# Kernel tuning notes

Measured on AMD Instinct MI355X. Metric: run time of the kernel, lower is better.

## Reference

```python
import jax, jax.numpy as jnp
import numpy as np

D_MODEL = 1024
N_HEADS = 16
HEAD_DIM = D_MODEL // N_HEADS  # 64
BASE = 10000.0
MAX_X, MAX_Y, MAX_Z = 32, 32, 8
NEG_INF = -1e9  # stand-in for float('-inf') in masked_fill; identical after softmax


def _split_dims(head_dim):
    n_pairs = head_dim // 2
    px = n_pairs // 3
    py = n_pairs // 3
    pz = n_pairs - px - py
    return px * 2, py * 2, pz * 2


def _cos_sin_table(dim, max_pos):
    # matches RotaryEmbedding3D._register_cache
    inv_freq = 1.0 / (BASE ** (np.arange(0, dim, 2, dtype=np.float32) / dim))
    t = np.arange(max_pos, dtype=np.float32)[:, None] * inv_freq  # [max_pos, dim/2]
    cos = np.repeat(np.cos(t), 2, axis=-1)  # repeat_interleave(2)
    sin = np.repeat(np.sin(t), 2, axis=-1)
    return jnp.asarray(cos), jnp.asarray(sin)


def _rotate_half(x):
    x1 = x[..., ::2]
    x2 = x[..., 1::2]
    return jnp.stack((-x2, x1), axis=-1).reshape(x.shape)


def setup_inputs() -> dict:
    key = jax.random.key(0)
    k1, k2, k3, k4, k5, k6 = jax.random.split(key, 6)
    B, S = 2, 2048
    hidden_states = jax.random.normal(k1, (B, S, D_MODEL), dtype=jnp.float32)
    w_qkv = jax.random.normal(k2, (D_MODEL, 3 * D_MODEL), dtype=jnp.float32) * 0.02
    w_out = jax.random.normal(k3, (D_MODEL, D_MODEL), dtype=jnp.float32) * 0.02
    px = jax.random.randint(k4, (B, S, 1), 0, MAX_X)
    py = jax.random.randint(k5, (B, S, 1), 0, MAX_Y)
    pz = jax.random.randint(k6, (B, S, 1), 0, MAX_Z)
    pos_xyz = jnp.concatenate([px, py, pz], axis=-1).astype(jnp.int64)
    causal_mask = jnp.triu(jnp.ones((S, S), dtype=bool), k=1)[None, None]  # [1,1,S,S]
    return {"hidden_states": hidden_states, "w_qkv": w_qkv, "w_out": w_out,
            "pos_xyz": pos_xyz, "causal_mask": causal_mask}


def reference(hidden_states, w_qkv, w_out, pos_xyz, causal_mask):
    B, S, D = hidden_states.shape
    H, Hd = N_HEADS, HEAD_DIM
    # fused QKV projection
    qkv = hidden_states @ w_qkv  # [B,S,3D]
    qkv = qkv.reshape(B, S, 3, H, Hd).transpose(2, 0, 3, 1, 4)  # [3,B,H,S,Hd]
    q, k, v = qkv[0], qkv[1], qkv[2]
    # 3D RoPE tables and lookups
    dx, dy, dz = _split_dims(Hd)
    cx, sx = _cos_sin_table(dx, MAX_X)
    cy, sy = _cos_sin_table(dy, MAX_Y)
    cz, sz = _cos_sin_table(dz, MAX_Z)
    ix = jnp.clip(pos_xyz[..., 0], 0, MAX_X - 1)
    iy = jnp.clip(pos_xyz[..., 1], 0, MAX_Y - 1)
    iz = jnp.clip(pos_xyz[..., 2], 0, MAX_Z - 1)
    cos = jnp.concatenate([cx[ix], cy[iy], cz[iz]], axis=-1)[:, None]  # [B,1,S,Hd]
    sin = jnp.concatenate([sx[ix], sy[iy], sz[iz]], axis=-1)[:, None]
    q = q * cos + _rotate_half(q) * sin
    k = k * cos + _rotate_half(k) * sin
    # SDPA with causal bias
    scale = Hd ** -0.5
    scores = jnp.einsum('bhqd,bhkd->bhqk', q, k) * scale
    scores = jnp.where(causal_mask, jnp.asarray(NEG_INF, scores.dtype), scores)
    probs = jax.nn.softmax(scores, axis=-1)
    attn = jnp.einsum('bhqk,bhkd->bhqd', probs, v)
    attn = attn.transpose(0, 2, 1, 3).reshape(B, S, D)
    return attn @ w_out
```

## Files before the change

### kernel.cpp

```cpp
#include <hip/hip_runtime.h>
#include <hip/hip_bf16.h>
#include <math.h>

typedef __bf16 bf16;
typedef __bf16 bf16x8 __attribute__((ext_vector_type(8)));
typedef float f32x4 __attribute__((ext_vector_type(4)));

#define SEQ 2048
#define NHEADS 16
#define HDIM 64
#define DM 1024
#define QKVW 3072

__device__ __forceinline__ void gload_lds16(const void* g, void* l) {
  __builtin_amdgcn_global_load_lds(
      (const __attribute__((address_space(1))) unsigned int*)g,
      (__attribute__((address_space(3))) unsigned int*)l, 16, 0, 0);
}

template <int CTRL>
__device__ __forceinline__ float dppmovf(float x) {
  return __builtin_bit_cast(
      float, __builtin_amdgcn_mov_dpp(__builtin_bit_cast(int, x), CTRL, 0xf,
                                      0xf, true));
}
__device__ __forceinline__ float rowsum16(float x) {
  x += dppmovf<0xB1>(x);
  x += dppmovf<0x4E>(x);
  x += dppmovf<0x124>(x);
  x += dppmovf<0x128>(x);
  return x;
}

__global__ __launch_bounds__(256) void prep(
    const float* __restrict__ hidden, const float* __restrict__ w_qkv,
    const float* __restrict__ w_out, const int* __restrict__ pos,
    bf16* __restrict__ hid_bf, bf16* __restrict__ wqkvT,
    bf16* __restrict__ woutT, float2* __restrict__ tbl) {
  __shared__ float tile[64][65];
  int idx = blockIdx.x, tid = threadIdx.x;
  if (idx < 2048) {
    int i = (idx * 256 + tid) * 8;
    float4 a = *(const float4*)(hidden + i);
    float4 b = *(const float4*)(hidden + i + 4);
    bf16x8 o;
    o[0] = (bf16)a.x; o[1] = (bf16)a.y; o[2] = (bf16)a.z; o[3] = (bf16)a.w;
    o[4] = (bf16)b.x; o[5] = (bf16)b.y; o[6] = (bf16)b.z; o[7] = (bf16)b.w;
    *(bf16x8*)(hid_bf + i) = o;
  } else if (idx < 3072) {
    const float* in; bf16* out; int R, C, t;
    if (idx < 2816) { t = idx - 2048; in = w_qkv; out = wqkvT; R = 1024; C = 3072; }
    else            { t = idx - 2816; in = w_out; out = woutT; R = 1024; C = 1024; }
    int nbx = C >> 6;
    int c0 = (t % nbx) * 64, r0 = (t / nbx) * 64;
    int col = tid & 63, rb = (tid >> 6) * 16;
#pragma unroll
    for (int i = 0; i < 16; ++i)
      tile[rb + i][col] = in[(size_t)(r0 + rb + i) * C + c0 + col];
    __syncthreads();
#pragma unroll
    for (int i = 0; i < 16; ++i)
      out[(size_t)(c0 + rb + i) * R + r0 + col] = (bf16)tile[col][rb + i];
  } else {
    const float LN1E4 = 9.210340371976184f;
    int gi = (idx - 3072) * 256 + tid;
    int m = gi >> 5, pr = gi & 31;
    int axis, d, iloc;
    if (pr < 10)      { axis = 0; d = 20; iloc = pr; }
    else if (pr < 20) { axis = 1; d = 20; iloc = pr - 10; }
    else              { axis = 2; d = 24; iloc = pr - 20; }
    int p = pos[m * 3 + axis];
    int pmax = (axis == 2) ? 7 : 31;
    p = p < 0 ? 0 : (p > pmax ? pmax : p);
    float invf = __expf(-((float)(2 * iloc) / (float)d) * LN1E4);
    float sn, cs;
    __sincosf((float)p * invf, &sn, &cs);
    tbl[gi] = make_float2(cs, sn);
  }
}

__global__ __launch_bounds__(256) void post_qkv(
    bf16* __restrict__ qkv, const float2* __restrict__ tbl,
    bf16* __restrict__ vT) {
  __shared__ bf16 btile[64][65];
  int idx = blockIdx.x, tid = threadIdx.x;
  if (idx < 2048) {
    int gi = idx * 256 + tid;
    int m = gi >> 7, seg = gi & 127;
    bf16* p = qkv + (size_t)m * QKVW + seg * 16;
    bf16x8 a = *(const bf16x8*)p;
    bf16x8 b2 = *(const bf16x8*)(p + 8);
    const float2* t = tbl + m * 32 + (((seg * 16) & 63) >> 1);
#pragma unroll
    for (int j = 0; j < 4; ++j) {
      float2 cs = t[j];
      float e = (float)a[2 * j], o = (float)a[2 * j + 1];
      a[2 * j]     = (bf16)(e * cs.x - o * cs.y);
      a[2 * j + 1] = (bf16)(o * cs.x + e * cs.y);
    }
#pragma unroll
    for (int j = 0; j < 4; ++j) {
      float2 cs = t[4 + j];
      float e = (float)b2[2 * j], o = (float)b2[2 * j + 1];
      b2[2 * j]     = (bf16)(e * cs.x - o * cs.y);
      b2[2 * j + 1] = (bf16)(o * cs.x + e * cs.y);
    }
    *(bf16x8*)p = a;
    *(bf16x8*)(p + 8) = b2;
  } else {
    int t = idx - 2048;
    int s0 = (t & 31) * 64, bh = t >> 5;
    int b = bh >> 4, h = bh & 15;
    const bf16* src = qkv + (size_t)(b * SEQ + s0) * QKVW + 2 * DM + h * 64;
    int col = tid & 63, rb = (tid >> 6) * 16;
#pragma unroll
    for (int i = 0; i < 16; ++i)
      btile[rb + i][col] = src[(size_t)(rb + i) * QKVW + col];
    __syncthreads();
    bf16* dst = vT + (size_t)bh * HDIM * SEQ + s0;
#pragma unroll
    for (int i = 0; i < 16; ++i)
      dst[(size_t)(rb + i) * SEQ + col] = btile[col][rb + i];
  }
}

__global__ __launch_bounds__(256) void gemm_bt(
    const bf16* __restrict__ A, const bf16* __restrict__ Bt,
    bf16* __restrict__ C, int M, int N, int K) {
  __shared__ __align__(16) bf16 a_lds[128 * 32];
  __shared__ __align__(16) bf16 b_lds[128 * 32];
  int tid = threadIdx.x;
  int wave = tid >> 6, lane = tid & 63;
  int quad = lane >> 4, l15 = lane & 15;
  int wm = wave >> 1, wn = wave & 1;

  int flat = blockIdx.y * gridDim.x + blockIdx.x;
  int mband = gridDim.y >> 3;
  int xcd = flat & 7, sidx = flat >> 3;
  int m0 = (xcd * mband + (sidx % mband)) * 128;
  int n0 = (sidx / mband) * 128;

  f32x4 acc[4][4] = {};

  for (int kt = 0; kt < K; kt += 32) {
    __syncthreads();
#pragma unroll
    for (int call = 0; call < 2; ++call) {
      int chunk = call * 256 + tid;
      int row = chunk >> 2, cc = (chunk & 3) * 8;
      gload_lds16(A + (size_t)(m0 + row) * K + kt + cc,
                  (char*)a_lds + call * 4096 + wave * 1024);
      gload_lds16(Bt + (size_t)(n0 + row) * K + kt + cc,
                  (char*)b_lds + call * 4096 + wave * 1024);
    }
    __syncthreads();
    bf16x8 af[4], bfr[4];
#pragma unroll
    for (int i = 0; i < 4; ++i) {
      af[i]  = *(const bf16x8*)(a_lds + (wm * 64 + i * 16 + l15) * 32 + quad * 8);
      bfr[i] = *(const bf16x8*)(b_lds + (wn * 64 + i * 16 + l15) * 32 + quad * 8);
    }
#pragma unroll
    for (int mi = 0; mi < 4; ++mi)
#pragma unroll
      for (int ni = 0; ni < 4; ++ni)
        acc[mi][ni] = __builtin_amdgcn_mfma_f32_16x16x32_bf16(
            af[mi], bfr[ni], acc[mi][ni], 0, 0, 0);
  }

#pragma unroll
  for (int mi = 0; mi < 4; ++mi) {
    int mb = m0 + wm * 64 + mi * 16 + quad * 4;
#pragma unroll
    for (int ni = 0; ni < 4; ++ni) {
      int n = n0 + wn * 64 + ni * 16 + l15;
#pragma unroll
      for (int r = 0; r < 4; ++r)
        C[(size_t)(mb + r) * N + n] = (bf16)acc[mi][ni][r];
    }
  }
}

__global__ __launch_bounds__(256) void gemm_bt64(
    const bf16* __restrict__ A, const bf16* __restrict__ Bt,
    float* __restrict__ C, int M, int N, int K) {
  __shared__ __align__(16) bf16 a_lds[64 * 32];
  __shared__ __align__(16) bf16 b_lds[128 * 32];
  int tid = threadIdx.x;
  int wave = tid >> 6, lane = tid & 63;
  int quad = lane >> 4, l15 = lane & 15;
  int wm = wave >> 1, wn = wave & 1;

  int flat = blockIdx.y * gridDim.x + blockIdx.x;
  int mband = gridDim.y >> 3;
  int xcd = flat & 7, sidx = flat >> 3;
  int m0 = (xcd * mband + (sidx % mband)) * 64;
  int n0 = (sidx / mband) * 128;

  f32x4 acc[2][4] = {};

  for (int kt = 0; kt < K; kt += 32) {
    __syncthreads();
    {
      int row = tid >> 2, cc = (tid & 3) * 8;
      gload_lds16(A + (size_t)(m0 + row) * K + kt + cc,
                  (char*)a_lds + wave * 1024);
    }
#pragma unroll
    for (int call = 0; call < 2; ++call) {
      int chunk = call * 256 + tid;
      int row = chunk >> 2, cc = (chunk & 3) * 8;
      gload_lds16(Bt + (size_t)(n0 + row) * K + kt + cc,
                  (char*)b_lds + call * 4096 + wave * 1024);
    }
    __syncthreads();
    bf16x8 af[2], bfr[4];
#pragma unroll
    for (int i = 0; i < 2; ++i)
      af[i] = *(const bf16x8*)(a_lds + (wm * 32 + i * 16 + l15) * 32 + quad * 8);
#pragma unroll
    for (int i = 0; i < 4; ++i)
      bfr[i] = *(const bf16x8*)(b_lds + (wn * 64 + i * 16 + l15) * 32 + quad * 8);
#pragma unroll
    for (int mi = 0; mi < 2; ++mi)
#pragma unroll
      for (int ni = 0; ni < 4; ++ni)
        acc[mi][ni] = __builtin_amdgcn_mfma_f32_16x16x32_bf16(
            af[mi], bfr[ni], acc[mi][ni], 0, 0, 0);
  }

#pragma unroll
  for (int mi = 0; mi < 2; ++mi) {
    int mb = m0 + wm * 32 + mi * 16 + quad * 4;
#pragma unroll
    for (int ni = 0; ni < 4; ++ni) {
      int n = n0 + wn * 64 + ni * 16 + l15;
#pragma unroll
      for (int r = 0; r < 4; ++r)
        C[(size_t)(mb + r) * N + n] = acc[mi][ni][r];
    }
  }
}

__global__ __launch_bounds__(256) void attn_fwd(
    const bf16* __restrict__ QKV, const bf16* __restrict__ VT,
    bf16* __restrict__ O) {
  __shared__ __align__(16) bf16 k_lds[2][64 * 72];
  __shared__ __align__(16) bf16 v_lds[2][64 * 72];
  __shared__ __align__(16) bf16 p_lds[4][16 * 72];
  const float C2 = 0.18033688011112042f;
  const float C3 = -5.770780163555854f;
  int tid = threadIdx.x;
  int wave = tid >> 6, lane = tid & 63;
  int quad = lane >> 4, l15 = lane & 15;
  int idx = blockIdx.x;
  int bh = idx & 31;
  int g = idx >> 5;
  int qt = (g < 16) ? (31 - g) : (g - 16);
  int q0 = qt * 64;
  int b = bh >> 4, h = bh & 15;
  const bf16* Qb = QKV + (size_t)b * SEQ * QKVW + h * 64;
  const bf16* Kb = Qb + DM;
  const bf16* VTb = VT + (size_t)bh * HDIM * SEQ;
  bf16* pw = p_lds[wave];

  const bf16* qr = Qb + (size_t)(q0 + wave * 16 + l15) * QKVW;
  bf16x8 qf0 = *(const bf16x8*)(qr + quad * 8);
  bf16x8 qf1 = *(const bf16x8*)(qr + 32 + quad * 8);

  int r0c = tid >> 3, off0 = (tid & 7) * 8;

  int niter = qt + 1;
  f32x4 o_acc[4] = {};
  float lsum[4] = {};
  int qrow[4];
#pragma unroll
  for (int r = 0; r < 4; ++r) qrow[r] = q0 + wave * 16 + quad * 4 + r;

  bf16x8 kpre0 = *(const bf16x8*)(Kb + (size_t)r0c * QKVW + off0);
  bf16x8 kpre1 = *(const bf16x8*)(Kb + (size_t)(r0c + 32) * QKVW + off0);
  bf16x8 vpre0 = *(const bf16x8*)(VTb + (size_t)r0c * SEQ + off0);
  bf16x8 vpre1 = *(const bf16x8*)(VTb + (size_t)(r0c + 32) * SEQ + off0);

  for (int tkv = 0; tkv < niter; ++tkv) {
    int kv0 = tkv * 64;
    bf16* kb = k_lds[tkv & 1];
    bf16* vb = v_lds[tkv & 1];
    *(bf16x8*)(kb + r0c * 72 + off0) = kpre0;
    *(bf16x8*)(kb + (r0c + 32) * 72 + off0) = kpre1;
    *(bf16x8*)(vb + r0c * 72 + off0) = vpre0;
    *(bf16x8*)(vb + (r0c + 32) * 72 + off0) = vpre1;
    __syncthreads();
    if (tkv + 1 < niter) {
      int kn = kv0 + 64;
      kpre0 = *(const bf16x8*)(Kb + (size_t)(kn + r0c) * QKVW + off0);
      kpre1 = *(const bf16x8*)(Kb + (size_t)(kn + r0c + 32) * QKVW + off0);
      vpre0 = *(const bf16x8*)(VTb + (size_t)r0c * SEQ + kn + off0);
      vpre1 = *(const bf16x8*)(VTb + (size_t)(r0c + 32) * SEQ + kn + off0);
    }
    f32x4 s_acc[4];
    __builtin_amdgcn_s_setprio(1);
#pragma unroll
    for (int nt = 0; nt < 4; ++nt) {
      const bf16* kr = kb + (nt * 16 + l15) * 72;
      bf16x8 kf0 = *(const bf16x8*)(kr + quad * 8);
      bf16x8 kf1 = *(const bf16x8*)(kr + 32 + quad * 8);
      f32x4 z = {};
      z = __builtin_amdgcn_mfma_f32_16x16x32_bf16(qf0, kf0, z, 0, 0, 0);
      z = __builtin_amdgcn_mfma_f32_16x16x32_bf16(qf1, kf1, z, 0, 0, 0);
      s_acc[nt] = z;
    }
    __builtin_amdgcn_s_setprio(0);
    if (tkv == qt) {
#pragma unroll
      for (int r = 0; r < 4; ++r) {
#pragma unroll
        for (int nt = 0; nt < 4; ++nt) {
          float p = __builtin_amdgcn_exp2f(s_acc[nt][r] * C2 + C3);
          if (kv0 + nt * 16 + l15 > qrow[r]) p = 0.f;
          lsum[r] += p;
          pw[(quad * 4 + r) * 72 + nt * 16 + l15] = (bf16)p;
        }
      }
    } else {
#pragma unroll
      for (int r = 0; r < 4; ++r) {
#pragma unroll
        for (int nt = 0; nt < 4; ++nt) {
          float p = __builtin_amdgcn_exp2f(s_acc[nt][r] * C2 + C3);
          lsum[r] += p;
          pw[(quad * 4 + r) * 72 + nt * 16 + l15] = (bf16)p;
        }
      }
    }
    __asm__ volatile("s_waitcnt lgkmcnt(0)" ::: "memory");
    bf16x8 pf0 = *(const bf16x8*)(pw + l15 * 72 + quad * 8);
    bf16x8 pf1 = *(const bf16x8*)(pw + l15 * 72 + 32 + quad * 8);
    __builtin_amdgcn_s_setprio(1);
#pragma unroll
    for (int nt = 0; nt < 4; ++nt) {
      const bf16* vr = vb + (nt * 16 + l15) * 72;
      bf16x8 vf0 = *(const bf16x8*)(vr + quad * 8);
      bf16x8 vf1 = *(const bf16x8*)(vr + 32 + quad * 8);
      o_acc[nt] = __builtin_amdgcn_mfma_f32_16x16x32_bf16(pf0, vf0, o_acc[nt], 0, 0, 0);
      o_acc[nt] = __builtin_amdgcn_mfma_f32_16x16x32_bf16(pf1, vf1, o_acc[nt], 0, 0, 0);
    }
    __builtin_amdgcn_s_setprio(0);
  }
#pragma unroll
  for (int r = 0; r < 4; ++r) {
    float inv = 1.f / rowsum16(lsum[r]);
    int sq = qrow[r];
#pragma unroll
    for (int nt = 0; nt < 4; ++nt)
      O[((size_t)(b * SEQ + sq)) * DM + h * HDIM + nt * 16 + l15] =
          (bf16)(o_acc[nt][r] * inv);
  }
}

extern "C" void kernel_launch(void* const* d_in, const int* in_sizes, int n_in,
                              void* d_out, int out_size, void* d_ws,
                              size_t ws_size, hipStream_t stream) {
  const float* hidden = (const float*)d_in[0];
  const float* w_qkv  = (const float*)d_in[1];
  const float* w_out  = (const float*)d_in[2];
  const int*   pos    = (const int*)d_in[3];
  float* out = (float*)d_out;

  char* ws = (char*)d_ws;
  bf16* wqkvT  = (bf16*)ws;  ws += (size_t)3072 * 1024 * 2;
  bf16* woutT  = (bf16*)ws;  ws += (size_t)1024 * 1024 * 2;
  bf16* hid_bf = (bf16*)ws;  ws += (size_t)4096 * 1024 * 2;
  bf16* qkv_ws = (bf16*)ws;  ws += (size_t)4096 * 3072 * 2;
  bf16* vT_ws  = (bf16*)ws;  ws += (size_t)32 * SEQ * HDIM * 2;
  float2* ropetbl = (float2*)ws;
  bf16* attn_ws = hid_bf;

  prep<<<dim3(3584), 256, 0, stream>>>(hidden, w_qkv, w_out, pos,
                                       hid_bf, wqkvT, woutT, ropetbl);
  gemm_bt<<<dim3(24, 32), 256, 0, stream>>>(
      hid_bf, wqkvT, qkv_ws, 4096, 3072, 1024);
  post_qkv<<<dim3(3072), 256, 0, stream>>>(qkv_ws, ropetbl, vT_ws);
  attn_fwd<<<dim3(1024), 256, 0, stream>>>(qkv_ws, vT_ws, attn_ws);
  gemm_bt64<<<dim3(8, 64), 256, 0, stream>>>(
      attn_ws, woutT, out, 4096, 1024, 1024);
}
```

Before: 200.1 us.

## Compute transposed scores to keep P in registers and skip the LDS round-trip

The QK^T MFMA now runs with its operands swapped, so each lane holds scores for one query across several keys. That layout lets the probabilities be packed straight into bf16 MFMA A-operands without writing P to shared memory and reading it back. V fragments are now read as split 4-element LDS loads to match the new k ordering, and the row-sum reduction moves from a DPP reduction to cross-quad shuffles. This removes per-tile LDS stores, a wait and reloads of P, at the cost of narrower V loads and possibly more bank conflicts.

Result: faster. 196.1 us (-2.0%).

```diff
diff --git a/kernel.cpp b/kernel.cpp
--- a/kernel.cpp
+++ b/kernel.cpp
@@ -3,8 +3,10 @@
 #include <math.h>
 
 typedef __bf16 bf16;
+typedef __bf16 bf16x4 __attribute__((ext_vector_type(4)));
 typedef __bf16 bf16x8 __attribute__((ext_vector_type(8)));
 typedef float f32x4 __attribute__((ext_vector_type(4)));
+typedef int i32x4 __attribute__((ext_vector_type(4)));
 
 #define SEQ 2048
 #define NHEADS 16
@@ -18,18 +20,10 @@
       (__attribute__((address_space(3))) unsigned int*)l, 16, 0, 0);
 }
 
-template <int CTRL>
-__device__ __forceinline__ float dppmovf(float x) {
-  return __builtin_bit_cast(
-      float, __builtin_amdgcn_mov_dpp(__builtin_bit_cast(int, x), CTRL, 0xf,
-                                      0xf, true));
-}
-__device__ __forceinline__ float rowsum16(float x) {
-  x += dppmovf<0xB1>(x);
-  x += dppmovf<0x4E>(x);
-  x += dppmovf<0x124>(x);
-  x += dppmovf<0x128>(x);
-  return x;
+__device__ __forceinline__ int pk2(float a, float b) {
+  union { __bf16 h; unsigned short u; } ua, ub;
+  ua.h = (__bf16)a; ub.h = (__bf16)b;
+  return (int)ua.u | ((int)ub.u << 16);
 }
 
 __global__ __launch_bounds__(256) void prep(
@@ -247,7 +241,6 @@
     bf16* __restrict__ O) {
   __shared__ __align__(16) bf16 k_lds[2][64 * 72];
   __shared__ __align__(16) bf16 v_lds[2][64 * 72];
-  __shared__ __align__(16) bf16 p_lds[4][16 * 72];
   const float C2 = 0.18033688011112042f;
   const float C3 = -5.770780163555854f;
   int tid = threadIdx.x;
@@ -262,20 +255,17 @@
   const bf16* Qb = QKV + (size_t)b * SEQ * QKVW + h * 64;
   const bf16* Kb = Qb + DM;
   const bf16* VTb = VT + (size_t)bh * HDIM * SEQ;
-  bf16* pw = p_lds[wave];
-
-  const bf16* qr = Qb + (size_t)(q0 + wave * 16 + l15) * QKVW;
+
+  int qg = q0 + wave * 16 + l15;
+  const bf16* qr = Qb + (size_t)qg * QKVW;
   bf16x8 qf0 = *(const bf16x8*)(qr + quad * 8);
   bf16x8 qf1 = *(const bf16x8*)(qr + 32 + quad * 8);
 
   int r0c = tid >> 3, off0 = (tid & 7) * 8;
 
   int niter = qt + 1;
-  f32x4 o_acc[4] = {};
-  float lsum[4] = {};
-  int qrow[4];
-#pragma unroll
-  for (int r = 0; r < 4; ++r) qrow[r] = q0 + wave * 16 + quad * 4 + r;
+  f32x4 oT[4] = {};
+  float lsum = 0.f;
 
   bf16x8 kpre0 = *(const bf16x8*)(Kb + (size_t)r0c * QKVW + off0);
   bf16x8 kpre1 = *(const bf16x8*)(Kb + (size_t)(r0c + 32) * QKVW + off0);
@@ -298,7 +288,7 @@
       vpre0 = *(const bf16x8*)(VTb + (size_t)r0c * SEQ + kn + off0);
       vpre1 = *(const bf16x8*)(VTb + (size_t)(r0c + 32) * SEQ + kn + off0);
     }
-    f32x4 s_acc[4];
+    f32x4 sT[4];
     __builtin_amdgcn_s_setprio(1);
 #pragma unroll
     for (int nt = 0; nt < 4; ++nt) {
@@ -306,55 +296,66 @@
       bf16x8 kf0 = *(const bf16x8*)(kr + quad * 8);
       bf16x8 kf1 = *(const bf16x8*)(kr + 32 + quad * 8);
       f32x4 z = {};
-      z = __builtin_amdgcn_mfma_f32_16x16x32_bf16(qf0, kf0, z, 0, 0, 0);
-      z = __builtin_amdgcn_mfma_f32_16x16x32_bf16(qf1, kf1, z, 0, 0, 0);
-      s_acc[nt] = z;
+      z = __builtin_amdgcn_mfma_f32_16x16x32_bf16(kf0, qf0, z, 0, 0, 0);
+      z = __builtin_amdgcn_mfma_f32_16x16x32_bf16(kf1, qf1, z, 0, 0, 0);
+      sT[nt] = z;
     }
     __builtin_amdgcn_s_setprio(0);
+    float pv[4][4];
     if (tkv == qt) {
 #pragma unroll
-      for (int r = 0; r < 4; ++r) {
-#pragma unroll
-        for (int nt = 0; nt < 4; ++nt) {
-          float p = __builtin_amdgcn_exp2f(s_acc[nt][r] * C2 + C3);
-          if (kv0 + nt * 16 + l15 > qrow[r]) p = 0.f;
-          lsum[r] += p;
-          pw[(quad * 4 + r) * 72 + nt * 16 + l15] = (bf16)p;
+      for (int nt = 0; nt < 4; ++nt)
+#pragma unroll
+        for (int r = 0; r < 4; ++r) {
+          float p = __builtin_amdgcn_exp2f(sT[nt][r] * C2 + C3);
+          int kvg = kv0 + nt * 16 + 4 * quad + r;
+          if (kvg > qg) p = 0.f;
+          pv[nt][r] = p;
+          lsum += p;
         }
-      }
     } else {
 #pragma unroll
-      for (int r = 0; r < 4; ++r) {
-#pragma unroll
-        for (int nt = 0; nt < 4; ++nt) {
-          float p = __builtin_amdgcn_exp2f(s_acc[nt][r] * C2 + C3);
-          lsum[r] += p;
-          pw[(quad * 4 + r) * 72 + nt * 16 + l15] = (bf16)p;
+      for (int nt = 0; nt < 4; ++nt)
+#pragma unroll
+        for (int r = 0; r < 4; ++r) {
+          float p = __builtin_amdgcn_exp2f(sT[nt][r] * C2 + C3);
+          pv[nt][r] = p;
+          lsum += p;
         }
-      }
-    }
-    __asm__ volatile("s_waitcnt lgkmcnt(0)" ::: "memory");
-    bf16x8 pf0 = *(const bf16x8*)(pw + l15 * 72 + quad * 8);
-    bf16x8 pf1 = *(const bf16x8*)(pw + l15 * 72 + 32 + quad * 8);
+    }
+    i32x4 w0 = {pk2(pv[0][0], pv[0][1]), pk2(pv[0][2], pv[0][3]),
+                pk2(pv[1][0], pv[1][1]), pk2(pv[1][2], pv[1][3])};
+    i32x4 w1 = {pk2(pv[2][0], pv[2][1]), pk2(pv[2][2], pv[2][3]),
+                pk2(pv[3][0], pv[3][1]), pk2(pv[3][2], pv[3][3])};
+    bf16x8 pa0 = __builtin_bit_cast(bf16x8, w0);
+    bf16x8 pa1 = __builtin_bit_cast(bf16x8, w1);
     __builtin_amdgcn_s_setprio(1);
 #pragma unroll
-    for (int nt = 0; nt < 4; ++nt) {
-      const bf16* vr = vb + (nt * 16 + l15) * 72;
-      bf16x8 vf0 = *(const bf16x8*)(vr + quad * 8);
-      bf16x8 vf1 = *(const bf16x8*)(vr + 32 + quad * 8);
-      o_acc[nt] = __builtin_amdgcn_mfma_f32_16x16x32_bf16(pf0, vf0, o_acc[nt], 0, 0, 0);
-      o_acc[nt] = __builtin_amdgcn_mfma_f32_16x16x32_bf16(pf1, vf1, o_acc[nt], 0, 0, 0);
+    for (int dt = 0; dt < 4; ++dt) {
+      const bf16* vd = vb + (dt * 16 + l15) * 72 + 4 * quad;
+      bf16x4 a0 = *(const bf16x4*)(vd);
+      bf16x4 a1 = *(const bf16x4*)(vd + 16);
+      bf16x8 vf0 = __builtin_shufflevector(a0, a1, 0, 1, 2, 3, 4, 5, 6, 7);
+      oT[dt] = __builtin_amdgcn_mfma_f32_16x16x32_bf16(pa0, vf0, oT[dt], 0, 0, 0);
+      bf16x4 b0 = *(const bf16x4*)(vd + 32);
+      bf16x4 b1 = *(const bf16x4*)(vd + 48);
+      bf16x8 vf1 = __builtin_shufflevector(b0, b1, 0, 1, 2, 3, 4, 5, 6, 7);
+      oT[dt] = __builtin_amdgcn_mfma_f32_16x16x32_bf16(pa1, vf1, oT[dt], 0, 0, 0);
     }
     __builtin_amdgcn_s_setprio(0);
   }
+  float t = lsum;
+  t += __shfl_xor(t, 16);
+  t += __shfl_xor(t, 32);
 #pragma unroll
   for (int r = 0; r < 4; ++r) {
-    float inv = 1.f / rowsum16(lsum[r]);
-    int sq = qrow[r];
-#pragma unroll
-    for (int nt = 0; nt < 4; ++nt)
-      O[((size_t)(b * SEQ + sq)) * DM + h * HDIM + nt * 16 + l15] =
-          (bf16)(o_acc[nt][r] * inv);
+    float Lr = __shfl(t, 4 * quad + r);
+    float inv = 1.f / Lr;
+    int sq = q0 + wave * 16 + 4 * quad + r;
+#pragma unroll
+    for (int dt = 0; dt < 4; ++dt)
+      O[(size_t)(b * SEQ + sq) * DM + h * HDIM + dt * 16 + l15] =
+          (bf16)(oT[dt][r] * inv);
   }
 }
 
```
